# Optimization experiments

Measured on AMD Instinct MI355X. Metric: run time of the kernel, lower is better.

The kernel has to match this reference:

```python
import jax, jax.numpy as jnp
import numpy as np

EPS = 1e-12  # torch F.normalize eps

def _l2norm(v, axis):
    n = jnp.sqrt(jnp.sum(v * v, axis=axis, keepdims=True))
    return v / jnp.maximum(n, EPS)

def setup_inputs() -> dict:
    key = jax.random.key(0)
    k1, k2, k3 = jax.random.split(key, 3)
    N, D, H, W, K = 32, 512, 56, 56, 64
    x = jax.random.normal(k1, (N, D, H, W), dtype=jnp.float32)
    conv_w = jax.random.normal(k2, (K, D), dtype=jnp.float32) * 0.05
    centroids = jax.random.uniform(k3, (K, D), dtype=jnp.float32)
    return {"x": x, "conv_w": conv_w, "centroids": centroids}

def reference(x, conv_w, centroids):
    N, D, H, W = x.shape
    K = centroids.shape[0]
    # descriptor-wise L2 normalization over channel dim
    x = _l2norm(x, axis=1)
    x_flat = x.reshape(N, D, H * W)                      # (N, D, P)
    # 1x1 conv == per-pixel linear map: (K,D) x (N,D,P) -> (N,K,P)
    logits = jnp.einsum('kd,ndp->nkp', conv_w, x_flat)
    soft_assign = jax.nn.softmax(logits, axis=1)         # softmax over clusters
    # vlad[n,k,:] = sum_p a[n,k,p] * (x[n,:,p] - c[k,:])
    #            = (a @ x^T)[n,k,:] - (sum_p a[n,k,p]) * c[k,:]
    agg = jnp.einsum('nkp,ndp->nkd', soft_assign, x_flat)           # (N, K, D)
    a_sum = jnp.sum(soft_assign, axis=2)                            # (N, K)
    vlad = agg - a_sum[:, :, None] * centroids[None, :, :]
    vlad = _l2norm(vlad, axis=2)        # intra-normalization per cluster
    vlad = vlad.reshape(N, K * D)
    vlad = _l2norm(vlad, axis=1)        # global L2 normalization
    return vlad
```

## Files before the change

kernel.cpp:

```cpp
#include <hip/hip_runtime.h>
#include <hip/hip_bf16.h>

typedef unsigned short u16;
typedef unsigned int u32;
typedef __bf16 bf16x8 __attribute__((ext_vector_type(8)));
typedef float f32x4 __attribute__((ext_vector_type(4)));

#define N_ 32
#define D_ 512
#define P_ 3136
#define K_ 64
#define NDP (D_ * P_)


__device__ __forceinline__ u16 f2bf(float f) {
  u32 u = __float_as_uint(f);
  return (u16)((u + 0x7fffu + ((u >> 16) & 1u)) >> 16);
}
__device__ __forceinline__ u32 pack2(float a, float b) {
  return (u32)f2bf(a) | ((u32)f2bf(b) << 16);
}

__global__ __launch_bounds__(256) void kw_kernel(const float* __restrict__ w,
                                                 u16* __restrict__ wbf) {
  int i = blockIdx.x * 256 + threadIdx.x;
  float4 v = ((const float4*)w)[i];
  ((uint2*)wbf)[i] = make_uint2(pack2(v.x, v.y), pack2(v.z, v.w));
}

__global__ __launch_bounds__(256, 1) void f_kernel(const float* __restrict__ x,
                                                   const u16* __restrict__ wbf,
                                                   float* __restrict__ agg,
                                                   float* __restrict__ a_sum) {
  __shared__ __align__(16) char xbuf[131072];
  __shared__ float a_stage[64][65];
  __shared__ float invn_s[64];
  __shared__ __align__(16) char a_bf[8192];

  const int t = threadIdx.x;
  const int lane = t & 63;
  const int w = t >> 6;
  const int c = lane & 15;
  const int q = lane >> 4;
  const int b = blockIdx.x;
  const int n = b >> 3;
  const int s = b & 7;
  const int tile0 = (s == 0) ? 0 : 7 + (s - 1) * 6;
  const int ntl = (s == 0) ? 7 : 6;
  const int rp = w * 16 + c;
  const int rpc = rp >> 2;
  const int rpo = (rp & 3) * 4;
  const int c7 = c & 7;

  const bf16x8* wrow = (const bf16x8*)wbf;
  const char* xgb = (const char*)(x + (size_t)n * NDP);

  f32x4 acc2[4][8];
#pragma unroll
  for (int m = 0; m < 4; ++m)
#pragma unroll
    for (int i = 0; i < 8; ++i) acc2[m][i] = (f32x4){0.f, 0.f, 0.f, 0.f};
  float ssum_acc = 0.f;

  for (int tt = 0; tt < ntl; ++tt) {
    const int p0 = (tile0 + tt) * 64;

#pragma unroll
    for (int i = 0; i < 32; ++i) {
      const int d = w * 128 + i * 4 + q;
      const char* src = xgb + ((size_t)d * P_ + p0) * 4 + ((c ^ (d & 7)) << 4);
      __builtin_amdgcn_global_load_lds(
          (const __attribute__((address_space(1))) void*)src,
          (__attribute__((address_space(3))) void*)(xbuf + w * 32768 + i * 1024),
          16, 0, 0);
    }
    __syncthreads();

    f32x4 acc[4];
#pragma unroll
    for (int m = 0; m < 4; ++m) acc[m] = (f32x4){0.f, 0.f, 0.f, 0.f};
    float sumsq = 0.f;
    bf16x8 pa[2][4];
#pragma unroll
    for (int m = 0; m < 4; ++m) {
      pa[0][m] = wrow[(m * 16 + c) * 64 + q];
      pa[1][m] = wrow[(m * 16 + c) * 64 + 4 + q];
    }
    float vc[8];
#pragma unroll
    for (int j = 0; j < 8; ++j)
      vc[j] = *(const float*)(xbuf + ((q * 8 + j) << 8) + ((rpc ^ j) << 4) + rpo);
#pragma unroll
    for (int st = 0; st < 16; ++st) {
      float vn[8];
      if (st < 15) {
#pragma unroll
        for (int j = 0; j < 8; ++j)
          vn[j] = *(const float*)(xbuf + (((st + 1) * 32 + q * 8 + j) << 8) +
                                  ((rpc ^ j) << 4) + rpo);
      }
      bf16x8 bfr;
#pragma unroll
      for (int j = 0; j < 8; ++j) {
        sumsq += vc[j] * vc[j];
        bfr[j] = (__bf16)vc[j];
      }
      bf16x8 nf[4];
      if (st < 14) {
#pragma unroll
        for (int m = 0; m < 4; ++m)
          nf[m] = wrow[(m * 16 + c) * 64 + (st + 2) * 4 + q];
      }
#pragma unroll
      for (int m = 0; m < 4; ++m)
        acc[m] = __builtin_amdgcn_mfma_f32_16x16x32_bf16(pa[st & 1][m], bfr, acc[m], 0, 0, 0);
      if (st < 14) {
#pragma unroll
        for (int m = 0; m < 4; ++m) pa[st & 1][m] = nf[m];
      }
      if (st < 15) {
#pragma unroll
        for (int j = 0; j < 8; ++j) vc[j] = vn[j];
      }
    }

    sumsq += __shfl_xor(sumsq, 16);
    sumsq += __shfl_xor(sumsq, 32);
    const float inv_p = 1.f / fmaxf(sqrtf(sumsq), 1e-12f);
    if (q == 0) invn_s[rp] = inv_p;

    float sc[4][4];
    float lmax = -3.0e38f;
#pragma unroll
    for (int m = 0; m < 4; ++m)
#pragma unroll
      for (int r = 0; r < 4; ++r) {
        float val = acc[m][r] * inv_p;
        sc[m][r] = val;
        lmax = fmaxf(lmax, val);
      }
    lmax = fmaxf(lmax, __shfl_xor(lmax, 16));
    lmax = fmaxf(lmax, __shfl_xor(lmax, 32));
    float lsum = 0.f;
#pragma unroll
    for (int m = 0; m < 4; ++m)
#pragma unroll
      for (int r = 0; r < 4; ++r) {
        float e = __expf(sc[m][r] - lmax);
        sc[m][r] = e;
        lsum += e;
      }
    lsum += __shfl_xor(lsum, 16);
    lsum += __shfl_xor(lsum, 32);
    const float rs = 1.f / lsum;
#pragma unroll
    for (int m = 0; m < 4; ++m)
#pragma unroll
      for (int r = 0; r < 4; ++r)
        a_stage[m * 16 + q * 4 + r][rp] = sc[m][r] * rs;
    __syncthreads();

    {
      const int k = t >> 2, pc4 = t & 3;
      float ssum = 0.f;
      u32 u[8];
#pragma unroll
      for (int jj = 0; jj < 8; ++jj) {
        int p = pc4 * 16 + jj * 2;
        float a0 = a_stage[k][p], a1 = a_stage[k][p + 1];
        ssum += a0 + a1;
        u[jj] = (u32)f2bf(a0 * invn_s[p]) | ((u32)f2bf(a1 * invn_s[p + 1]) << 16);
      }
      *(uint4*)(a_bf + k * 128 + (((pc4 * 2) ^ (k & 7)) << 4)) =
          make_uint4(u[0], u[1], u[2], u[3]);
      *(uint4*)(a_bf + k * 128 + (((pc4 * 2 + 1) ^ (k & 7)) << 4)) =
          make_uint4(u[4], u[5], u[6], u[7]);
      ssum_acc += ssum;
    }
    __syncthreads();

#pragma unroll
    for (int st = 0; st < 2; ++st) {
      bf16x8 afr[4];
#pragma unroll
      for (int m = 0; m < 4; ++m)
        afr[m] = *(const bf16x8*)(a_bf + (m * 16 + c) * 128 +
                                  (((st * 4 + q) ^ c7) << 4));
      const int pc0 = st * 8 + q * 2;
#pragma unroll
      for (int nt = 0; nt < 8; ++nt) {
        const int d = w * 128 + nt * 16 + c;
        f32x4 b0 = *(const f32x4*)(xbuf + (d << 8) + ((pc0 ^ c7) << 4));
        f32x4 b1 = *(const f32x4*)(xbuf + (d << 8) + (((pc0 + 1) ^ c7) << 4));
        bf16x8 bfr;
#pragma unroll
        for (int i4 = 0; i4 < 4; ++i4) {
          bfr[i4] = (__bf16)b0[i4];
          bfr[4 + i4] = (__bf16)b1[i4];
        }
#pragma unroll
        for (int m = 0; m < 4; ++m)
          acc2[m][nt] = __builtin_amdgcn_mfma_f32_16x16x32_bf16(afr[m], bfr, acc2[m][nt], 0, 0, 0);
      }
    }
    __syncthreads();
  }

  float* ob = agg + ((size_t)s * 32 + n) * (K_ * D_);
#pragma unroll
  for (int m = 0; m < 4; ++m)
#pragma unroll
    for (int nt = 0; nt < 8; ++nt)
#pragma unroll
      for (int r = 0; r < 4; ++r)
        ob[(m * 16 + q * 4 + r) * D_ + w * 128 + nt * 16 + c] = acc2[m][nt][r];
  ssum_acc += __shfl_xor(ssum_acc, 1);
  ssum_acc += __shfl_xor(ssum_acc, 2);
  if ((t & 3) == 0) atomicAdd(&a_sum[n * 64 + (t >> 2)], ssum_acc);
}

__global__ __launch_bounds__(256) void k3a_kernel(const float* __restrict__ agg,
                                                  const float* __restrict__ a_sum,
                                                  const float* __restrict__ cent,
                                                  float* __restrict__ out,
                                                  float* __restrict__ rowsq) {
  const int b = blockIdx.x;
  const int n = b >> 4, kg = b & 15;
  const int t = threadIdx.x;
  const int lane = t & 63, w = t >> 6;
  const int k = kg * 4 + w;
  const float* ab = agg + ((size_t)n * 64 + k) * 512 + lane * 8;
  float v[8];
#pragma unroll
  for (int j = 0; j < 8; ++j) v[j] = 0.f;
#pragma unroll
  for (int pp = 0; pp < 8; ++pp) {
    const float4* p4 = (const float4*)(ab + (size_t)pp * 32 * (K_ * D_));
    float4 r0 = p4[0], r1 = p4[1];
    v[0] += r0.x; v[1] += r0.y; v[2] += r0.z; v[3] += r0.w;
    v[4] += r1.x; v[5] += r1.y; v[6] += r1.z; v[7] += r1.w;
  }
  const float asum = a_sum[n * 64 + k];
  const float4* c4 = (const float4*)(cent + k * 512 + lane * 8);
  float4 c0 = c4[0], c1 = c4[1];
  v[0] -= asum * c0.x; v[1] -= asum * c0.y; v[2] -= asum * c0.z; v[3] -= asum * c0.w;
  v[4] -= asum * c1.x; v[5] -= asum * c1.y; v[6] -= asum * c1.z; v[7] -= asum * c1.w;
  float ssq = 0.f;
#pragma unroll
  for (int j = 0; j < 8; ++j) ssq += v[j] * v[j];
  ssq += __shfl_xor(ssq, 1);  ssq += __shfl_xor(ssq, 2);  ssq += __shfl_xor(ssq, 4);
  ssq += __shfl_xor(ssq, 8);  ssq += __shfl_xor(ssq, 16); ssq += __shfl_xor(ssq, 32);
  float4* o4 = (float4*)(out + (size_t)n * 32768 + k * 512 + lane * 8);
  o4[0] = make_float4(v[0], v[1], v[2], v[3]);
  o4[1] = make_float4(v[4], v[5], v[6], v[7]);
  if (lane == 0) rowsq[n * 64 + k] = ssq;
}

__global__ __launch_bounds__(256) void k3b_kernel(const float* __restrict__ rowsq,
                                                  float* __restrict__ out) {
  __shared__ float invr_s[64];
  __shared__ float gi_s;
  const int n = blockIdx.x >> 3;
  const int seg = blockIdx.x & 7;
  const int t = threadIdx.x;
  if (t < 64) {
    float r = rowsq[n * 64 + t];
    float ri = 1.f / fmaxf(sqrtf(r), 1e-12f);
    invr_s[t] = ri;
    float g = r * ri * ri;
    g += __shfl_xor(g, 1); g += __shfl_xor(g, 2); g += __shfl_xor(g, 4);
    g += __shfl_xor(g, 8); g += __shfl_xor(g, 16); g += __shfl_xor(g, 32);
    if (t == 0) gi_s = 1.f / fmaxf(sqrtf(g), 1e-12f);
  }
  __syncthreads();
  const int e0 = seg * 4096 + t * 16;
  const float sc = invr_s[e0 >> 9] * gi_s;
  float4* o4 = (float4*)(out + (size_t)n * 32768 + e0);
#pragma unroll
  for (int i = 0; i < 4; ++i) {
    float4 vv = o4[i];
    vv.x *= sc; vv.y *= sc; vv.z *= sc; vv.w *= sc;
    o4[i] = vv;
  }
}

extern "C" void kernel_launch(void* const* d_in, const int* in_sizes, int n_in,
                              void* d_out, int out_size, void* d_ws, size_t ws_size,
                              hipStream_t stream) {
  (void)in_sizes; (void)n_in; (void)out_size; (void)ws_size;
  const float* x    = (const float*)d_in[0];
  const float* cw   = (const float*)d_in[1];
  const float* cent = (const float*)d_in[2];
  float* out = (float*)d_out;
  char* ws = (char*)d_ws;
  u16*   wbf   = (u16*)(ws);
  float* a_sum = (float*)(ws + 65536);
  float* agg   = (float*)(ws + 73728);
  float* rowsq = (float*)(ws + 33628160);

  hipMemsetAsync(a_sum, 0, 64 * 32 * sizeof(float), stream);
  kw_kernel<<<32, 256, 0, stream>>>(cw, wbf);
  f_kernel<<<256, 256, 0, stream>>>(x, wbf, agg, a_sum);
  k3a_kernel<<<512, 256, 0, stream>>>(agg, a_sum, cent, out, rowsq);
  k3b_kernel<<<256, 256, 0, stream>>>(rowsq, out);
}
```

Baseline: 368.4 us.

## Split fused NetVLAD kernel across 512 threads with two-half softmax merge

Doubles the workgroup to 512 threads (8 waves). Each half of the waves computes logits for 32 of the 64 clusters, and a cross-half max/sum merge through shared memory completes the softmax. This removes the a_stage transpose buffer and writes the bf16 assignments directly. The aggregation GEMM is split so each wave covers 64 of the channels instead of 128, which halves its accumulator registers. The LDS swizzle changes from XOR to a rotation to match the new layout. The goal is more waves in flight to hide the global-to-LDS load latency per tile. In exchange the cluster-logit work is duplicated across waves, and the scalar 2-byte LDS stores and extra shuffles may add cost.

```diff
diff --git a/kernel.cpp b/kernel.cpp
--- a/kernel.cpp
+++ b/kernel.cpp
@@ -28,76 +28,89 @@
   ((uint2*)wbf)[i] = make_uint2(pack2(v.x, v.y), pack2(v.z, v.w));
 }
 
-__global__ __launch_bounds__(256, 1) void f_kernel(const float* __restrict__ x,
+__global__ __launch_bounds__(512, 2) void f_kernel(const float* __restrict__ x,
                                                    const u16* __restrict__ wbf,
                                                    float* __restrict__ agg,
                                                    float* __restrict__ a_sum) {
   __shared__ __align__(16) char xbuf[131072];
-  __shared__ float a_stage[64][65];
-  __shared__ float invn_s[64];
   __shared__ __align__(16) char a_bf[8192];
+  __shared__ float pmax[2][64];
+  __shared__ float psum[2][64];
 
   const int t = threadIdx.x;
   const int lane = t & 63;
   const int w = t >> 6;
   const int c = lane & 15;
   const int q = lane >> 4;
+  const int h = w >> 2;
+  const int g = w & 3;
   const int b = blockIdx.x;
   const int n = b >> 3;
   const int s = b & 7;
   const int tile0 = (s == 0) ? 0 : 7 + (s - 1) * 6;
   const int ntl = (s == 0) ? 7 : 6;
-  const int rp = w * 16 + c;
+  const int rp = g * 16 + c;
   const int rpc = rp >> 2;
   const int rpo = (rp & 3) * 4;
   const int c7 = c & 7;
+  const int kb = h * 32;
 
   const bf16x8* wrow = (const bf16x8*)wbf;
   const char* xgb = (const char*)(x + (size_t)n * NDP);
 
-  f32x4 acc2[4][8];
-#pragma unroll
-  for (int m = 0; m < 4; ++m)
-#pragma unroll
-    for (int i = 0; i < 8; ++i) acc2[m][i] = (f32x4){0.f, 0.f, 0.f, 0.f};
-  float ssum_acc = 0.f;
+  f32x4 acc2[4][4];
+#pragma unroll
+  for (int m4 = 0; m4 < 4; ++m4)
+#pragma unroll
+    for (int nt = 0; nt < 4; ++nt) acc2[m4][nt] = (f32x4){0.f, 0.f, 0.f, 0.f};
+  float ssum_acc[2][4];
+#pragma unroll
+  for (int m = 0; m < 2; ++m)
+#pragma unroll
+    for (int r = 0; r < 4; ++r) ssum_acc[m][r] = 0.f;
 
   for (int tt = 0; tt < ntl; ++tt) {
     const int p0 = (tile0 + tt) * 64;
 
 #pragma unroll
-    for (int i = 0; i < 32; ++i) {
-      const int d = w * 128 + i * 4 + q;
-      const char* src = xgb + ((size_t)d * P_ + p0) * 4 + ((c ^ (d & 7)) << 4);
+    for (int i = 0; i < 16; ++i) {
+      const int dq = w * 64 + i * 4 + q;
+      const int f = ((i * 4 + q) & 7) + 2 * ((i >> 1) & 3);
+      const int gch = (c - f) & 15;
+      const char* src = xgb + ((size_t)dq * P_ + p0) * 4 + (gch << 4);
       __builtin_amdgcn_global_load_lds(
           (const __attribute__((address_space(1))) void*)src,
-          (__attribute__((address_space(3))) void*)(xbuf + w * 32768 + i * 1024),
+          (__attribute__((address_space(3))) void*)(xbuf + w * 16384 + i * 1024),
           16, 0, 0);
     }
     __syncthreads();
 
-    f32x4 acc[4];
-#pragma unroll
-    for (int m = 0; m < 4; ++m) acc[m] = (f32x4){0.f, 0.f, 0.f, 0.f};
+    f32x4 acc1[2];
+    acc1[0] = (f32x4){0.f, 0.f, 0.f, 0.f};
+    acc1[1] = (f32x4){0.f, 0.f, 0.f, 0.f};
     float sumsq = 0.f;
-    bf16x8 pa[2][4];
-#pragma unroll
-    for (int m = 0; m < 4; ++m) {
-      pa[0][m] = wrow[(m * 16 + c) * 64 + q];
-      pa[1][m] = wrow[(m * 16 + c) * 64 + 4 + q];
+    bf16x8 pa[2][2];
+#pragma unroll
+    for (int m = 0; m < 2; ++m) {
+      pa[0][m] = wrow[(kb + m * 16 + c) * 64 + q];
+      pa[1][m] = wrow[(kb + m * 16 + c) * 64 + 4 + q];
     }
     float vc[8];
 #pragma unroll
-    for (int j = 0; j < 8; ++j)
-      vc[j] = *(const float*)(xbuf + ((q * 8 + j) << 8) + ((rpc ^ j) << 4) + rpo);
+    for (int j = 0; j < 8; ++j) {
+      const int ch = (rpc + j + 2 * q) & 15;
+      vc[j] = *(const float*)(xbuf + ((q * 8 + j) << 8) + (ch << 4) + rpo);
+    }
 #pragma unroll
     for (int st = 0; st < 16; ++st) {
       float vn[8];
       if (st < 15) {
 #pragma unroll
-        for (int j = 0; j < 8; ++j)
+        for (int j = 0; j < 8; ++j) {
+          const int ch = (rpc + j + 2 * q) & 15;
           vn[j] = *(const float*)(xbuf + (((st + 1) * 32 + q * 8 + j) << 8) +
-                                  ((rpc ^ j) << 4) + rpo);
+                                  (ch << 4) + rpo);
+        }
       }
       bf16x8 bfr;
 #pragma unroll
@@ -105,18 +118,17 @@
         sumsq += vc[j] * vc[j];
         bfr[j] = (__bf16)vc[j];
       }
-      bf16x8 nf[4];
+      bf16x8 nf[2];
       if (st < 14) {
 #pragma unroll
-        for (int m = 0; m < 4; ++m)
-          nf[m] = wrow[(m * 16 + c) * 64 + (st + 2) * 4 + q];
-      }
-#pragma unroll
-      for (int m = 0; m < 4; ++m)
-        acc[m] = __builtin_amdgcn_mfma_f32_16x16x32_bf16(pa[st & 1][m], bfr, acc[m], 0, 0, 0);
+        for (int m = 0; m < 2; ++m)
+          nf[m] = wrow[(kb + m * 16 + c) * 64 + (st + 2) * 4 + q];
+      }
+      acc1[0] = __builtin_amdgcn_mfma_f32_16x16x32_bf16(pa[st & 1][0], bfr, acc1[0], 0, 0, 0);
+      acc1[1] = __builtin_amdgcn_mfma_f32_16x16x32_bf16(pa[st & 1][1], bfr, acc1[1], 0, 0, 0);
       if (st < 14) {
-#pragma unroll
-        for (int m = 0; m < 4; ++m) pa[st & 1][m] = nf[m];
+        pa[st & 1][0] = nf[0];
+        pa[st & 1][1] = nf[1];
       }
       if (st < 15) {
 #pragma unroll
@@ -127,71 +139,68 @@
     sumsq += __shfl_xor(sumsq, 16);
     sumsq += __shfl_xor(sumsq, 32);
     const float inv_p = 1.f / fmaxf(sqrtf(sumsq), 1e-12f);
-    if (q == 0) invn_s[rp] = inv_p;
-
-    float sc[4][4];
+
+    float scv[2][4];
     float lmax = -3.0e38f;
 #pragma unroll
-    for (int m = 0; m < 4; ++m)
+    for (int m = 0; m < 2; ++m)
 #pragma unroll
       for (int r = 0; r < 4; ++r) {
-        float val = acc[m][r] * inv_p;
-        sc[m][r] = val;
+        float val = acc1[m][r] * inv_p;
+        scv[m][r] = val;
         lmax = fmaxf(lmax, val);
       }
     lmax = fmaxf(lmax, __shfl_xor(lmax, 16));
     lmax = fmaxf(lmax, __shfl_xor(lmax, 32));
     float lsum = 0.f;
 #pragma unroll
-    for (int m = 0; m < 4; ++m)
+    for (int m = 0; m < 2; ++m)
 #pragma unroll
       for (int r = 0; r < 4; ++r) {
-        float e = __expf(sc[m][r] - lmax);
-        sc[m][r] = e;
+        float e = __expf(scv[m][r] - lmax);
+        scv[m][r] = e;
         lsum += e;
       }
     lsum += __shfl_xor(lsum, 16);
     lsum += __shfl_xor(lsum, 32);
-    const float rs = 1.f / lsum;
-#pragma unroll
-    for (int m = 0; m < 4; ++m)
-#pragma unroll
-      for (int r = 0; r < 4; ++r)
-        a_stage[m * 16 + q * 4 + r][rp] = sc[m][r] * rs;
+    if (q == 0) {
+      pmax[h][rp] = lmax;
+      psum[h][rp] = lsum;
+    }
     __syncthreads();
-
-    {
-      const int k = t >> 2, pc4 = t & 3;
-      float ssum = 0.f;
-      u32 u[8];
-#pragma unroll
-      for (int jj = 0; jj < 8; ++jj) {
-        int p = pc4 * 16 + jj * 2;
-        float a0 = a_stage[k][p], a1 = a_stage[k][p + 1];
-        ssum += a0 + a1;
-        u[jj] = (u32)f2bf(a0 * invn_s[p]) | ((u32)f2bf(a1 * invn_s[p + 1]) << 16);
-      }
-      *(uint4*)(a_bf + k * 128 + (((pc4 * 2) ^ (k & 7)) << 4)) =
-          make_uint4(u[0], u[1], u[2], u[3]);
-      *(uint4*)(a_bf + k * 128 + (((pc4 * 2 + 1) ^ (k & 7)) << 4)) =
-          make_uint4(u[4], u[5], u[6], u[7]);
-      ssum_acc += ssum;
-    }
+    const float m0 = pmax[0][rp], m1 = pmax[1][rp];
+    const float M = fmaxf(m0, m1);
+    const float S = psum[0][rp] * __expf(m0 - M) + psum[1][rp] * __expf(m1 - M);
+    const float factor = __expf(lmax - M) / S;
+
+#pragma unroll
+    for (int m = 0; m < 2; ++m)
+#pragma unroll
+      for (int r = 0; r < 4; ++r) {
+        const float a = scv[m][r] * factor;
+        ssum_acc[m][r] += a;
+        const int k = kb + m * 16 + q * 4 + r;
+        const int chA = (g * 2 + (c >> 3)) ^ (k & 7);
+        *(u16*)(a_bf + k * 128 + (chA << 4) + (c7 << 1)) = f2bf(a * inv_p);
+      }
     __syncthreads();
 
 #pragma unroll
     for (int st = 0; st < 2; ++st) {
       bf16x8 afr[4];
 #pragma unroll
-      for (int m = 0; m < 4; ++m)
-        afr[m] = *(const bf16x8*)(a_bf + (m * 16 + c) * 128 +
-                                  (((st * 4 + q) ^ c7) << 4));
+      for (int m4 = 0; m4 < 4; ++m4)
+        afr[m4] = *(const bf16x8*)(a_bf + (m4 * 16 + c) * 128 +
+                                   (((st * 4 + q) ^ c7) << 4));
       const int pc0 = st * 8 + q * 2;
 #pragma unroll
-      for (int nt = 0; nt < 8; ++nt) {
-        const int d = w * 128 + nt * 16 + c;
-        f32x4 b0 = *(const f32x4*)(xbuf + (d << 8) + ((pc0 ^ c7) << 4));
-        f32x4 b1 = *(const f32x4*)(xbuf + (d << 8) + (((pc0 + 1) ^ c7) << 4));
+      for (int nt = 0; nt < 4; ++nt) {
+        const int d = w * 64 + nt * 16 + c;
+        const int f = (d & 7) + 2 * ((d >> 3) & 3);
+        const int ch0 = (pc0 + f) & 15;
+        const int ch1 = (pc0 + 1 + f) & 15;
+        f32x4 b0 = *(const f32x4*)(xbuf + (d << 8) + (ch0 << 4));
+        f32x4 b1 = *(const f32x4*)(xbuf + (d << 8) + (ch1 << 4));
         bf16x8 bfr;
 #pragma unroll
         for (int i4 = 0; i4 < 4; ++i4) {
@@ -199,8 +208,8 @@
           bfr[4 + i4] = (__bf16)b1[i4];
         }
 #pragma unroll
-        for (int m = 0; m < 4; ++m)
-          acc2[m][nt] = __builtin_amdgcn_mfma_f32_16x16x32_bf16(afr[m], bfr, acc2[m][nt], 0, 0, 0);
+        for (int m4 = 0; m4 < 4; ++m4)
+          acc2[m4][nt] = __builtin_amdgcn_mfma_f32_16x16x32_bf16(afr[m4], bfr, acc2[m4][nt], 0, 0, 0);
       }
     }
     __syncthreads();
@@ -208,15 +217,23 @@
 
   float* ob = agg + ((size_t)s * 32 + n) * (K_ * D_);
 #pragma unroll
-  for (int m = 0; m < 4; ++m)
-#pragma unroll
-    for (int nt = 0; nt < 8; ++nt)
+  for (int m4 = 0; m4 < 4; ++m4)
+#pragma unroll
+    for (int nt = 0; nt < 4; ++nt)
 #pragma unroll
       for (int r = 0; r < 4; ++r)
-        ob[(m * 16 + q * 4 + r) * D_ + w * 128 + nt * 16 + c] = acc2[m][nt][r];
-  ssum_acc += __shfl_xor(ssum_acc, 1);
-  ssum_acc += __shfl_xor(ssum_acc, 2);
-  if ((t & 3) == 0) atomicAdd(&a_sum[n * 64 + (t >> 2)], ssum_acc);
+        ob[(m4 * 16 + q * 4 + r) * D_ + w * 64 + nt * 16 + c] = acc2[m4][nt][r];
+#pragma unroll
+  for (int m = 0; m < 2; ++m)
+#pragma unroll
+    for (int r = 0; r < 4; ++r) {
+      float v = ssum_acc[m][r];
+      v += __shfl_xor(v, 1);
+      v += __shfl_xor(v, 2);
+      v += __shfl_xor(v, 4);
+      v += __shfl_xor(v, 8);
+      if (c == 0) atomicAdd(&a_sum[n * 64 + kb + m * 16 + q * 4 + r], v);
+    }
 }
 
 __global__ __launch_bounds__(256) void k3a_kernel(const float* __restrict__ agg,
@@ -300,7 +317,7 @@
 
   hipMemsetAsync(a_sum, 0, 64 * 32 * sizeof(float), stream);
   kw_kernel<<<32, 256, 0, stream>>>(cw, wbf);
-  f_kernel<<<256, 256, 0, stream>>>(x, wbf, agg, a_sum);
+  f_kernel<<<256, 512, 0, stream>>>(x, wbf, agg, a_sum);
   k3a_kernel<<<512, 256, 0, stream>>>(agg, a_sum, cent, out, rowsq);
   k3b_kernel<<<256, 256, 0, stream>>>(rowsq, out);
 }
```

After: 393.6 us. +6.8%, slower.
